# Optimization experiments

Hardware: AMD Instinct MI355X
Metric: run time of the kernel (lower is better)

The kernel has to match this reference:

```python
import jax, jax.numpy as jnp
import numpy as np

ALPHA = 0.25
GAMMA = 2.0
W_CLASS, W_BBOX, W_GIOU, W_EMBED = 1.0, 1.0, 1.0, 0.5
EPS = 1e-8


def box_cxcywh_to_xyxy(b):
    cx, cy, w, h = b[..., 0], b[..., 1], b[..., 2], b[..., 3]
    return jnp.stack([cx - 0.5 * w, cy - 0.5 * h, cx + 0.5 * w, cy + 0.5 * h], axis=-1)


def generalized_box_iou(boxes1, boxes2):
    # boxes1 [N,4], boxes2 [M,4] in xyxy -> [N,M]
    area1 = (boxes1[:, 2] - boxes1[:, 0]) * (boxes1[:, 3] - boxes1[:, 1])
    area2 = (boxes2[:, 2] - boxes2[:, 0]) * (boxes2[:, 3] - boxes2[:, 1])
    lt = jnp.maximum(boxes1[:, None, :2], boxes2[None, :, :2])  # [N,M,2]
    rb = jnp.minimum(boxes1[:, None, 2:], boxes2[None, :, 2:])
    wh = jnp.clip(rb - lt, 0.0)
    inter = wh[..., 0] * wh[..., 1]
    union = area1[:, None] + area2[None, :] - inter
    iou = inter / union
    lt_e = jnp.minimum(boxes1[:, None, :2], boxes2[None, :, :2])
    rb_e = jnp.maximum(boxes1[:, None, 2:], boxes2[None, :, 2:])
    wh_e = jnp.clip(rb_e - lt_e, 0.0)
    area_e = wh_e[..., 0] * wh_e[..., 1]
    return iou - (area_e - union) / area_e


def setup_inputs() -> dict:
    key = jax.random.key(0)
    ks = jax.random.split(key, 6)
    B, Q, C, D, M = 16, 1024, 91, 512, 1600
    pred_logits = jax.random.normal(ks[0], (B, Q, C), dtype=jnp.float32)
    pred_boxes = jax.random.uniform(ks[1], (B, Q, 4), dtype=jnp.float32)
    pred_embed = jax.random.normal(ks[2], (B, Q, D), dtype=jnp.float32)
    text_embeddings = jax.random.normal(ks[3], (C, D), dtype=jnp.float32)
    tgt_ids = jax.random.randint(ks[4], (M,), 0, C, dtype=jnp.int64 if jax.config.jax_enable_x64 else jnp.int32)
    tgt_bbox = jax.random.uniform(ks[5], (M, 4), dtype=jnp.float32)
    return {
        'pred_logits': pred_logits,
        'pred_boxes': pred_boxes,
        'pred_embed': pred_embed,
        'text_embeddings': text_embeddings,
        'tgt_ids': tgt_ids,
        'tgt_bbox': tgt_bbox,
    }


def reference(pred_logits, pred_boxes, pred_embed, text_embeddings, tgt_ids, tgt_bbox):
    B, Q, _ = pred_logits.shape
    N = B * Q
    # --- focal class cost on gathered target-class columns: [N, M]
    logits = pred_logits.reshape(N, -1)
    p = jax.nn.sigmoid(logits[:, tgt_ids])
    pos_cost = ALPHA * (1.0 - p) ** GAMMA * (-jnp.log(p + EPS))
    neg_cost = (1.0 - ALPHA) * p ** GAMMA * (-jnp.log(1.0 - p + EPS))
    cost_class = pos_cost - neg_cost
    # --- L1 box cost (cdist, p=1): [N, M]
    out_bbox = pred_boxes.reshape(N, 4)
    cost_bbox = jnp.sum(jnp.abs(out_bbox[:, None, :] - tgt_bbox[None, :, :]), axis=-1)
    # --- GIoU cost: [N, M]
    cost_giou = -generalized_box_iou(box_cxcywh_to_xyxy(out_bbox), box_cxcywh_to_xyxy(tgt_bbox))
    # --- embedding cosine cost: [N, M]
    v = pred_embed.reshape(N, -1)
    v = v / jnp.linalg.norm(v, axis=1, keepdims=True)
    te = text_embeddings[tgt_ids]  # [M, D]
    cost_embed = 1.0 - v @ te.T
    C = W_BBOX * cost_bbox + W_CLASS * cost_class + W_GIOU * cost_giou + W_EMBED * cost_embed
    return C.reshape(B, Q, -1)
```

## Files before the change

kernel.cpp:

```cpp
#include <hip/hip_runtime.h>
#include <hip/hip_bf16.h>

using bf16x8 = __attribute__((ext_vector_type(8))) short;
using f32x4  = __attribute__((ext_vector_type(4))) float;
using f32x2  = __attribute__((ext_vector_type(2))) float;

__device__ __forceinline__ unsigned short f2bf(float x) {
    unsigned int u = __float_as_uint(x);
    return (unsigned short)((u + 0x7FFFu + ((u >> 16) & 1u)) >> 16);
}

__global__ __launch_bounds__(256)
void k_prep(const float* __restrict__ te, unsigned short* __restrict__ te_bf) {
    const int r = blockIdx.x;
    for (int i = threadIdx.x; i < 512; i += 256) {
        const float v = (r < 91) ? te[(size_t)r * 512 + i] : 0.f;
        te_bf[(size_t)r * 512 + i] = f2bf(v);
    }
}

__device__ __forceinline__ float cost_core(
    float px0, float py0, float px1, float py1,
    float pcx, float pcy, float pw, float ph, float pa,
    float tx0, float ty0, float tx1, float ty1,
    float tcx, float tcy, float tw, float th, float ta, float cc)
{
    float res, t0, t1, t2, t3, t4, t5;
    asm("v_min_f32 %[t0], %[px1], %[tx1]\n\t"
        "v_max_f32 %[t1], %[px0], %[tx0]\n\t"
        "v_sub_f32 %[t0], %[t0], %[t1]\n\t"
        "v_min_f32 %[t1], %[py1], %[ty1]\n\t"
        "v_max_f32 %[t2], %[py0], %[ty0]\n\t"
        "v_sub_f32 %[t1], %[t1], %[t2]\n\t"
        "v_max_f32 %[t2], 0, %[t0]\n\t"
        "v_max_f32 %[t3], 0, %[t1]\n\t"
        "v_mul_f32 %[t4], %[t2], %[t3]\n\t"
        "v_add_f32 %[t2], %[pw], %[tw]\n\t"
        "v_sub_f32 %[t2], %[t2], %[t0]\n\t"
        "v_add_f32 %[t3], %[ph], %[th]\n\t"
        "v_sub_f32 %[t3], %[t3], %[t1]\n\t"
        "v_mul_f32 %[t0], %[t2], %[t3]\n\t"
        "v_add_f32 %[t1], %[pa], %[ta]\n\t"
        "v_sub_f32 %[t1], %[t1], %[t4]\n\t"
        "v_sub_f32 %[t2], %[t0], %[t1]\n\t"
        "v_mul_f32 %[t3], %[t1], %[t2]\n\t"
        "v_fma_f32 %[t2], %[t4], %[t0], -%[t3]\n\t"
        "v_mul_f32 %[t3], %[t1], %[t0]\n\t"
        "v_rcp_f32 %[t3], %[t3]\n\t"
        "v_sub_f32 %[t0], %[pcx], %[tcx]\n\t"
        "v_sub_f32 %[t1], %[pcy], %[tcy]\n\t"
        "v_add_f32 %[t4], |%[t0]|, |%[t1]|\n\t"
        "v_sub_f32 %[t0], %[pw], %[tw]\n\t"
        "v_sub_f32 %[t1], %[ph], %[th]\n\t"
        "v_add_f32 %[t5], |%[t0]|, |%[t1]|\n\t"
        "v_add_f32 %[t4], %[t4], %[t5]\n\t"
        "v_add_f32 %[t4], %[t4], %[cc]\n\t"
        "v_fma_f32 %[res], -%[t2], %[t3], %[t4]"
        : [res]"=v"(res), [t0]"=&v"(t0), [t1]"=&v"(t1), [t2]"=&v"(t2),
          [t3]"=&v"(t3), [t4]"=&v"(t4), [t5]"=&v"(t5)
        : [px0]"v"(px0), [py0]"v"(py0), [px1]"v"(px1), [py1]"v"(py1),
          [pcx]"v"(pcx), [pcy]"v"(pcy), [pw]"v"(pw), [ph]"v"(ph), [pa]"v"(pa),
          [tx0]"v"(tx0), [ty0]"v"(ty0), [tx1]"v"(tx1), [ty1]"v"(ty1),
          [tcx]"v"(tcx), [tcy]"v"(tcy), [tw]"v"(tw), [th]"v"(th), [ta]"v"(ta),
          [cc]"v"(cc));
    return res;
}

__global__ __launch_bounds__(256, 5)
void k_fused(const float* __restrict__ logits,
             const float* __restrict__ pboxes,
             const float* __restrict__ embed,
             const unsigned short* __restrict__ te_bf,
             const int* __restrict__ tids,
             const float* __restrict__ tboxes,
             float* __restrict__ out)
{
    __shared__ float accs[4][1536];
    __shared__ float sq_s[4][16];
    __shared__ float cc_s[1536];
    __shared__ float p_s[16 * 12];

    const int tid  = threadIdx.x;
    const int lane = tid & 63;
    const int wv   = tid >> 6;
    const int r16  = lane & 15;
    const int q    = lane >> 4;
    const int n0   = blockIdx.x * 16;

    if (tid < 16) {
        const float4 b = *(const float4*)(pboxes + (size_t)(n0 + tid) * 4);
        float* p = &p_s[tid * 12];
        p[0] = b.x; p[1] = b.y; p[2] = b.z; p[3] = b.w;
        p[4] = __builtin_fmaf(-0.5f, b.z, b.x);
        p[5] = __builtin_fmaf(-0.5f, b.w, b.y);
        p[6] = __builtin_fmaf( 0.5f, b.z, b.x);
        p[7] = __builtin_fmaf( 0.5f, b.w, b.y);
        p[8] = b.z * b.w;
    }

    const float* arow = embed + (size_t)(n0 + r16) * 512 + wv * 128 + q * 8;
    float4 A[8];
#pragma unroll
    for (int ks = 0; ks < 4; ++ks) {
        A[2 * ks]     = *(const float4*)(arow + ks * 32);
        A[2 * ks + 1] = *(const float4*)(arow + ks * 32 + 4);
    }

    float sumsq = 0.f;
    union { unsigned int uw[4]; bf16x8 v; } cvt[4];
#pragma unroll
    for (int ks = 0; ks < 4; ++ks) {
        const float4 a0 = A[2 * ks], a1 = A[2 * ks + 1];
        sumsq = __builtin_fmaf(a0.x, a0.x, sumsq);
        sumsq = __builtin_fmaf(a0.y, a0.y, sumsq);
        sumsq = __builtin_fmaf(a0.z, a0.z, sumsq);
        sumsq = __builtin_fmaf(a0.w, a0.w, sumsq);
        sumsq = __builtin_fmaf(a1.x, a1.x, sumsq);
        sumsq = __builtin_fmaf(a1.y, a1.y, sumsq);
        sumsq = __builtin_fmaf(a1.z, a1.z, sumsq);
        sumsq = __builtin_fmaf(a1.w, a1.w, sumsq);
        asm("v_cvt_pk_bf16_f32 %0, %1, %2" : "=v"(cvt[ks].uw[0]) : "v"(a0.x), "v"(a0.y));
        asm("v_cvt_pk_bf16_f32 %0, %1, %2" : "=v"(cvt[ks].uw[1]) : "v"(a0.z), "v"(a0.w));
        asm("v_cvt_pk_bf16_f32 %0, %1, %2" : "=v"(cvt[ks].uw[2]) : "v"(a1.x), "v"(a1.y));
        asm("v_cvt_pk_bf16_f32 %0, %1, %2" : "=v"(cvt[ks].uw[3]) : "v"(a1.z), "v"(a1.w));
    }

    f32x4 acc[6];
#pragma unroll
    for (int ct = 0; ct < 6; ++ct) {
        const bf16x8* bbase = (const bf16x8*)(te_bf + (size_t)(ct * 16 + r16) * 512
                                              + wv * 128 + q * 8);
        const bf16x8 b0 = bbase[0], b1 = bbase[4], b2 = bbase[8], b3 = bbase[12];
        f32x4 a = (f32x4){0.f, 0.f, 0.f, 0.f};
        a = __builtin_amdgcn_mfma_f32_16x16x32_bf16(cvt[0].v, b0, a, 0, 0, 0);
        a = __builtin_amdgcn_mfma_f32_16x16x32_bf16(cvt[1].v, b1, a, 0, 0, 0);
        a = __builtin_amdgcn_mfma_f32_16x16x32_bf16(cvt[2].v, b2, a, 0, 0, 0);
        a = __builtin_amdgcn_mfma_f32_16x16x32_bf16(cvt[3].v, b3, a, 0, 0, 0);
        acc[ct] = a;
    }

    sumsq += __shfl_xor(sumsq, 16);
    sumsq += __shfl_xor(sumsq, 32);
    if (lane < 16) sq_s[wv][r16] = sumsq;

#pragma unroll
    for (int ct = 0; ct < 6; ++ct)
#pragma unroll
        for (int j = 0; j < 4; ++j)
            accs[wv][(q * 4 + j) * 96 + ct * 16 + r16] = acc[ct][j];
    __syncthreads();

#pragma unroll
    for (int i = 0; i < 6; ++i) {
        const int e = tid + i * 256;
        const int row = e / 96, col = e - row * 96;
        float v = 0.f;
        if (col < 91) {
            const float dot = accs[0][e] + accs[1][e] + accs[2][e] + accs[3][e];
            const float rn = rsqrtf(sq_s[0][row] + sq_s[1][row]
                                  + sq_s[2][row] + sq_s[3][row]);
            const float x = logits[(size_t)(n0 + row) * 91 + col];
            const float p = 1.f / (1.f + __expf(-x));
            const float pos = 0.25f * (1.f - p) * (1.f - p) * (-__logf(p + 1e-8f));
            const float neg = 0.75f * p * p * (-__logf(1.f - p + 1e-8f));
            v = (pos - neg) + 0.5f - 0.5f * dot * rn;
        }
        cc_s[e] = v;
    }
    __syncthreads();

    const int r4 = wv * 4;
    float4 P0r[4], P1r[4];
    float  par[4];
#pragma unroll
    for (int r = 0; r < 4; ++r) {
        const float* pr = &p_s[(r4 + r) * 12];
        P0r[r] = *(const float4*)pr;
        P1r[r] = *(const float4*)(pr + 4);
        par[r] = pr[8];
    }

#pragma unroll
    for (int mc = 0; mc < 13; ++mc) {
        const int m  = mc * 128 + lane * 2;
        const bool valid = (m < 1600);
        const int mr = valid ? m : 1598;

        const float4 b0 = *(const float4*)(tboxes + (size_t)mr * 4);
        const float4 b1 = *(const float4*)(tboxes + (size_t)(mr + 1) * 4);
        const int2  idv = *(const int2*)(tids + mr);
        const int ids[2] = {idv.x, idv.y};

        float tcx[2], tcy[2], tw[2], th[2];
        float tx0[2], ty0[2], tx1[2], ty1[2], ta[2];
        const float4 bb[2] = {b0, b1};
#pragma unroll
        for (int j = 0; j < 2; ++j) {
            tcx[j] = bb[j].x; tcy[j] = bb[j].y; tw[j] = bb[j].z; th[j] = bb[j].w;
            tx0[j] = __builtin_fmaf(-0.5f, tw[j], tcx[j]);
            ty0[j] = __builtin_fmaf(-0.5f, th[j], tcy[j]);
            tx1[j] = __builtin_fmaf( 0.5f, tw[j], tcx[j]);
            ty1[j] = __builtin_fmaf( 0.5f, th[j], tcy[j]);
            ta[j]  = tw[j] * th[j];
        }

#pragma unroll
        for (int r = 0; r < 4; ++r) {
            const int nl = r4 + r;
            const float* ccrow = &cc_s[nl * 96];
            float res[2];
#pragma unroll
            for (int j = 0; j < 2; ++j) {
                res[j] = cost_core(P1r[r].x, P1r[r].y, P1r[r].z, P1r[r].w,
                                   P0r[r].x, P0r[r].y, P0r[r].z, P0r[r].w, par[r],
                                   tx0[j], ty0[j], tx1[j], ty1[j],
                                   tcx[j], tcy[j], tw[j], th[j], ta[j],
                                   ccrow[ids[j]]);
            }
            if (valid) {
                f32x2 r2 = {res[0], res[1]};
                *(f32x2*)(out + (size_t)(n0 + nl) * 1600 + m) = r2;
            }
        }
    }
}

extern "C" void kernel_launch(void* const* d_in, const int* in_sizes, int n_in,
                              void* d_out, int out_size, void* d_ws, size_t ws_size,
                              hipStream_t stream) {
    const float* pred_logits = (const float*)d_in[0];
    const float* pred_boxes  = (const float*)d_in[1];
    const float* pred_embed  = (const float*)d_in[2];
    const float* text_emb    = (const float*)d_in[3];
    const int*   tgt_ids     = (const int*)d_in[4];
    const float* tgt_bbox    = (const float*)d_in[5];
    float* out = (float*)d_out;

    unsigned short* te_bf = (unsigned short*)d_ws;

    k_prep<<<96, 256, 0, stream>>>(text_emb, te_bf);
    k_fused<<<1024, 256, 0, stream>>>(pred_logits, pred_boxes, pred_embed,
                                      te_bf, tgt_ids, tgt_bbox, out);
}
```

Baseline: 51.47 us.

## Process two 16-row tiles per block and prefetch the second tile's inputs

Each block now handles 32 prediction rows as two sequential 16-row tiles, halving the grid to 512 blocks. The embedding and logits for the second tile are loaded while the first tile's output phase runs, to hide global load latency behind the store-heavy box-cost loop. Launch bounds drop from 5 to 2 blocks per SM, which permits more registers for the extra prefetch buffers. The risks are lower occupancy, an extra barrier per tile, and fewer blocks to spread across the CUs.

Measured after the change: 53.42 us. 1.04x slower.

```diff
diff --git a/kernel.cpp b/kernel.cpp
--- a/kernel.cpp
+++ b/kernel.cpp
@@ -66,7 +66,7 @@
     return res;
 }
 
-__global__ __launch_bounds__(256, 5)
+__global__ __launch_bounds__(256, 2)
 void k_fused(const float* __restrict__ logits,
              const float* __restrict__ pboxes,
              const float* __restrict__ embed,
@@ -78,17 +78,17 @@
     __shared__ float accs[4][1536];
     __shared__ float sq_s[4][16];
     __shared__ float cc_s[1536];
-    __shared__ float p_s[16 * 12];
+    __shared__ float p_s[32 * 12];
 
     const int tid  = threadIdx.x;
     const int lane = tid & 63;
     const int wv   = tid >> 6;
     const int r16  = lane & 15;
     const int q    = lane >> 4;
-    const int n0   = blockIdx.x * 16;
-
-    if (tid < 16) {
-        const float4 b = *(const float4*)(pboxes + (size_t)(n0 + tid) * 4);
+    const int nb   = blockIdx.x * 32;
+
+    if (tid < 32) {
+        const float4 b = *(const float4*)(pboxes + (size_t)(nb + tid) * 4);
         float* p = &p_s[tid * 12];
         p[0] = b.x; p[1] = b.y; p[2] = b.z; p[3] = b.w;
         p[4] = __builtin_fmaf(-0.5f, b.z, b.x);
@@ -98,130 +98,160 @@
         p[8] = b.z * b.w;
     }
 
-    const float* arow = embed + (size_t)(n0 + r16) * 512 + wv * 128 + q * 8;
-    float4 A[8];
-#pragma unroll
-    for (int ks = 0; ks < 4; ++ks) {
-        A[2 * ks]     = *(const float4*)(arow + ks * 32);
-        A[2 * ks + 1] = *(const float4*)(arow + ks * 32 + 4);
-    }
-
-    float sumsq = 0.f;
-    union { unsigned int uw[4]; bf16x8 v; } cvt[4];
-#pragma unroll
-    for (int ks = 0; ks < 4; ++ks) {
-        const float4 a0 = A[2 * ks], a1 = A[2 * ks + 1];
-        sumsq = __builtin_fmaf(a0.x, a0.x, sumsq);
-        sumsq = __builtin_fmaf(a0.y, a0.y, sumsq);
-        sumsq = __builtin_fmaf(a0.z, a0.z, sumsq);
-        sumsq = __builtin_fmaf(a0.w, a0.w, sumsq);
-        sumsq = __builtin_fmaf(a1.x, a1.x, sumsq);
-        sumsq = __builtin_fmaf(a1.y, a1.y, sumsq);
-        sumsq = __builtin_fmaf(a1.z, a1.z, sumsq);
-        sumsq = __builtin_fmaf(a1.w, a1.w, sumsq);
-        asm("v_cvt_pk_bf16_f32 %0, %1, %2" : "=v"(cvt[ks].uw[0]) : "v"(a0.x), "v"(a0.y));
-        asm("v_cvt_pk_bf16_f32 %0, %1, %2" : "=v"(cvt[ks].uw[1]) : "v"(a0.z), "v"(a0.w));
-        asm("v_cvt_pk_bf16_f32 %0, %1, %2" : "=v"(cvt[ks].uw[2]) : "v"(a1.x), "v"(a1.y));
-        asm("v_cvt_pk_bf16_f32 %0, %1, %2" : "=v"(cvt[ks].uw[3]) : "v"(a1.z), "v"(a1.w));
-    }
-
-    f32x4 acc[6];
-#pragma unroll
-    for (int ct = 0; ct < 6; ++ct) {
-        const bf16x8* bbase = (const bf16x8*)(te_bf + (size_t)(ct * 16 + r16) * 512
-                                              + wv * 128 + q * 8);
-        const bf16x8 b0 = bbase[0], b1 = bbase[4], b2 = bbase[8], b3 = bbase[12];
-        f32x4 a = (f32x4){0.f, 0.f, 0.f, 0.f};
-        a = __builtin_amdgcn_mfma_f32_16x16x32_bf16(cvt[0].v, b0, a, 0, 0, 0);
-        a = __builtin_amdgcn_mfma_f32_16x16x32_bf16(cvt[1].v, b1, a, 0, 0, 0);
-        a = __builtin_amdgcn_mfma_f32_16x16x32_bf16(cvt[2].v, b2, a, 0, 0, 0);
-        a = __builtin_amdgcn_mfma_f32_16x16x32_bf16(cvt[3].v, b3, a, 0, 0, 0);
-        acc[ct] = a;
-    }
-
-    sumsq += __shfl_xor(sumsq, 16);
-    sumsq += __shfl_xor(sumsq, 32);
-    if (lane < 16) sq_s[wv][r16] = sumsq;
-
-#pragma unroll
-    for (int ct = 0; ct < 6; ++ct)
-#pragma unroll
-        for (int j = 0; j < 4; ++j)
-            accs[wv][(q * 4 + j) * 96 + ct * 16 + r16] = acc[ct][j];
-    __syncthreads();
-
-#pragma unroll
-    for (int i = 0; i < 6; ++i) {
-        const int e = tid + i * 256;
-        const int row = e / 96, col = e - row * 96;
-        float v = 0.f;
-        if (col < 91) {
-            const float dot = accs[0][e] + accs[1][e] + accs[2][e] + accs[3][e];
-            const float rn = rsqrtf(sq_s[0][row] + sq_s[1][row]
-                                  + sq_s[2][row] + sq_s[3][row]);
-            const float x = logits[(size_t)(n0 + row) * 91 + col];
-            const float p = 1.f / (1.f + __expf(-x));
-            const float pos = 0.25f * (1.f - p) * (1.f - p) * (-__logf(p + 1e-8f));
-            const float neg = 0.75f * p * p * (-__logf(1.f - p + 1e-8f));
-            v = (pos - neg) + 0.5f - 0.5f * dot * rn;
-        }
-        cc_s[e] = v;
-    }
-    __syncthreads();
-
-    const int r4 = wv * 4;
-    float4 P0r[4], P1r[4];
-    float  par[4];
-#pragma unroll
-    for (int r = 0; r < 4; ++r) {
-        const float* pr = &p_s[(r4 + r) * 12];
-        P0r[r] = *(const float4*)pr;
-        P1r[r] = *(const float4*)(pr + 4);
-        par[r] = pr[8];
-    }
-
-#pragma unroll
-    for (int mc = 0; mc < 13; ++mc) {
-        const int m  = mc * 128 + lane * 2;
-        const bool valid = (m < 1600);
-        const int mr = valid ? m : 1598;
-
-        const float4 b0 = *(const float4*)(tboxes + (size_t)mr * 4);
-        const float4 b1 = *(const float4*)(tboxes + (size_t)(mr + 1) * 4);
-        const int2  idv = *(const int2*)(tids + mr);
-        const int ids[2] = {idv.x, idv.y};
-
-        float tcx[2], tcy[2], tw[2], th[2];
-        float tx0[2], ty0[2], tx1[2], ty1[2], ta[2];
-        const float4 bb[2] = {b0, b1};
-#pragma unroll
-        for (int j = 0; j < 2; ++j) {
-            tcx[j] = bb[j].x; tcy[j] = bb[j].y; tw[j] = bb[j].z; th[j] = bb[j].w;
-            tx0[j] = __builtin_fmaf(-0.5f, tw[j], tcx[j]);
-            ty0[j] = __builtin_fmaf(-0.5f, th[j], tcy[j]);
-            tx1[j] = __builtin_fmaf( 0.5f, tw[j], tcx[j]);
-            ty1[j] = __builtin_fmaf( 0.5f, th[j], tcy[j]);
-            ta[j]  = tw[j] * th[j];
-        }
-
+    float4 A[2][8];
+    float  lg[2][6];
+    {
+        const float* arow = embed + (size_t)(nb + r16) * 512 + wv * 128 + q * 8;
+#pragma unroll
+        for (int ks = 0; ks < 4; ++ks) {
+            A[0][2 * ks]     = *(const float4*)(arow + ks * 32);
+            A[0][2 * ks + 1] = *(const float4*)(arow + ks * 32 + 4);
+        }
+#pragma unroll
+        for (int i = 0; i < 6; ++i) {
+            const int e = tid + i * 256;
+            const int row = e / 96, col = e - row * 96;
+            lg[0][i] = (col < 91) ? logits[(size_t)(nb + row) * 91 + col] : 0.f;
+        }
+    }
+
+#pragma unroll
+    for (int tt = 0; tt < 2; ++tt) {
+        const int n0 = nb + tt * 16;
+
+        float sumsq = 0.f;
+        union { unsigned int uw[4]; bf16x8 v; } cvt[4];
+#pragma unroll
+        for (int ks = 0; ks < 4; ++ks) {
+            const float4 a0 = A[tt][2 * ks], a1 = A[tt][2 * ks + 1];
+            sumsq = __builtin_fmaf(a0.x, a0.x, sumsq);
+            sumsq = __builtin_fmaf(a0.y, a0.y, sumsq);
+            sumsq = __builtin_fmaf(a0.z, a0.z, sumsq);
+            sumsq = __builtin_fmaf(a0.w, a0.w, sumsq);
+            sumsq = __builtin_fmaf(a1.x, a1.x, sumsq);
+            sumsq = __builtin_fmaf(a1.y, a1.y, sumsq);
+            sumsq = __builtin_fmaf(a1.z, a1.z, sumsq);
+            sumsq = __builtin_fmaf(a1.w, a1.w, sumsq);
+            asm("v_cvt_pk_bf16_f32 %0, %1, %2" : "=v"(cvt[ks].uw[0]) : "v"(a0.x), "v"(a0.y));
+            asm("v_cvt_pk_bf16_f32 %0, %1, %2" : "=v"(cvt[ks].uw[1]) : "v"(a0.z), "v"(a0.w));
+            asm("v_cvt_pk_bf16_f32 %0, %1, %2" : "=v"(cvt[ks].uw[2]) : "v"(a1.x), "v"(a1.y));
+            asm("v_cvt_pk_bf16_f32 %0, %1, %2" : "=v"(cvt[ks].uw[3]) : "v"(a1.z), "v"(a1.w));
+        }
+
+        f32x4 acc[6];
+#pragma unroll
+        for (int ct = 0; ct < 6; ++ct) {
+            const bf16x8* bbase = (const bf16x8*)(te_bf + (size_t)(ct * 16 + r16) * 512
+                                                  + wv * 128 + q * 8);
+            const bf16x8 b0 = bbase[0], b1 = bbase[4], b2 = bbase[8], b3 = bbase[12];
+            f32x4 a = (f32x4){0.f, 0.f, 0.f, 0.f};
+            a = __builtin_amdgcn_mfma_f32_16x16x32_bf16(cvt[0].v, b0, a, 0, 0, 0);
+            a = __builtin_amdgcn_mfma_f32_16x16x32_bf16(cvt[1].v, b1, a, 0, 0, 0);
+            a = __builtin_amdgcn_mfma_f32_16x16x32_bf16(cvt[2].v, b2, a, 0, 0, 0);
+            a = __builtin_amdgcn_mfma_f32_16x16x32_bf16(cvt[3].v, b3, a, 0, 0, 0);
+            acc[ct] = a;
+        }
+
+        sumsq += __shfl_xor(sumsq, 16);
+        sumsq += __shfl_xor(sumsq, 32);
+        if (lane < 16) sq_s[wv][r16] = sumsq;
+
+#pragma unroll
+        for (int ct = 0; ct < 6; ++ct)
+#pragma unroll
+            for (int j = 0; j < 4; ++j)
+                accs[wv][(q * 4 + j) * 96 + ct * 16 + r16] = acc[ct][j];
+        __syncthreads();
+
+#pragma unroll
+        for (int i = 0; i < 6; ++i) {
+            const int e = tid + i * 256;
+            const int row = e / 96, col = e - row * 96;
+            float v = 0.f;
+            if (col < 91) {
+                const float dot = accs[0][e] + accs[1][e] + accs[2][e] + accs[3][e];
+                const float rn = rsqrtf(sq_s[0][row] + sq_s[1][row]
+                                      + sq_s[2][row] + sq_s[3][row]);
+                const float x = lg[tt][i];
+                const float p = 1.f / (1.f + __expf(-x));
+                const float pos = 0.25f * (1.f - p) * (1.f - p) * (-__logf(p + 1e-8f));
+                const float neg = 0.75f * p * p * (-__logf(1.f - p + 1e-8f));
+                v = (pos - neg) + 0.5f - 0.5f * dot * rn;
+            }
+            cc_s[e] = v;
+        }
+        __syncthreads();
+
+        if (tt == 0) {
+            const float* arow = embed + (size_t)(nb + 16 + r16) * 512 + wv * 128 + q * 8;
+#pragma unroll
+            for (int ks = 0; ks < 4; ++ks) {
+                A[1][2 * ks]     = *(const float4*)(arow + ks * 32);
+                A[1][2 * ks + 1] = *(const float4*)(arow + ks * 32 + 4);
+            }
+#pragma unroll
+            for (int i = 0; i < 6; ++i) {
+                const int e = tid + i * 256;
+                const int row = e / 96, col = e - row * 96;
+                lg[1][i] = (col < 91) ? logits[(size_t)(nb + 16 + row) * 91 + col] : 0.f;
+            }
+        }
+
+        const int r4 = wv * 4;
+        float4 P0r[4], P1r[4];
+        float  par[4];
 #pragma unroll
         for (int r = 0; r < 4; ++r) {
-            const int nl = r4 + r;
-            const float* ccrow = &cc_s[nl * 96];
-            float res[2];
+            const float* pr = &p_s[(tt * 16 + r4 + r) * 12];
+            P0r[r] = *(const float4*)pr;
+            P1r[r] = *(const float4*)(pr + 4);
+            par[r] = pr[8];
+        }
+
+#pragma unroll
+        for (int mc = 0; mc < 13; ++mc) {
+            const int m  = mc * 128 + lane * 2;
+            const bool valid = (m < 1600);
+            const int mr = valid ? m : 1598;
+
+            const float4 b0 = *(const float4*)(tboxes + (size_t)mr * 4);
+            const float4 b1 = *(const float4*)(tboxes + (size_t)(mr + 1) * 4);
+            const int2  idv = *(const int2*)(tids + mr);
+            const int ids[2] = {idv.x, idv.y};
+
+            float tcx[2], tcy[2], tw[2], th[2];
+            float tx0[2], ty0[2], tx1[2], ty1[2], ta[2];
+            const float4 bb[2] = {b0, b1};
 #pragma unroll
             for (int j = 0; j < 2; ++j) {
-                res[j] = cost_core(P1r[r].x, P1r[r].y, P1r[r].z, P1r[r].w,
-                                   P0r[r].x, P0r[r].y, P0r[r].z, P0r[r].w, par[r],
-                                   tx0[j], ty0[j], tx1[j], ty1[j],
-                                   tcx[j], tcy[j], tw[j], th[j], ta[j],
-                                   ccrow[ids[j]]);
-            }
-            if (valid) {
-                f32x2 r2 = {res[0], res[1]};
-                *(f32x2*)(out + (size_t)(n0 + nl) * 1600 + m) = r2;
-            }
-        }
+                tcx[j] = bb[j].x; tcy[j] = bb[j].y; tw[j] = bb[j].z; th[j] = bb[j].w;
+                tx0[j] = __builtin_fmaf(-0.5f, tw[j], tcx[j]);
+                ty0[j] = __builtin_fmaf(-0.5f, th[j], tcy[j]);
+                tx1[j] = __builtin_fmaf( 0.5f, tw[j], tcx[j]);
+                ty1[j] = __builtin_fmaf( 0.5f, th[j], tcy[j]);
+                ta[j]  = tw[j] * th[j];
+            }
+
+#pragma unroll
+            for (int r = 0; r < 4; ++r) {
+                const int nl = r4 + r;
+                const float* ccrow = &cc_s[nl * 96];
+                float res[2];
+#pragma unroll
+                for (int j = 0; j < 2; ++j) {
+                    res[j] = cost_core(P1r[r].x, P1r[r].y, P1r[r].z, P1r[r].w,
+                                       P0r[r].x, P0r[r].y, P0r[r].z, P0r[r].w, par[r],
+                                       tx0[j], ty0[j], tx1[j], ty1[j],
+                                       tcx[j], tcy[j], tw[j], th[j], ta[j],
+                                       ccrow[ids[j]]);
+                }
+                if (valid) {
+                    f32x2 r2 = {res[0], res[1]};
+                    *(f32x2*)(out + (size_t)(n0 + nl) * 1600 + m) = r2;
+                }
+            }
+        }
+        __syncthreads();
     }
 }
 
@@ -239,6 +269,6 @@
     unsigned short* te_bf = (unsigned short*)d_ws;
 
     k_prep<<<96, 256, 0, stream>>>(text_emb, te_bf);
-    k_fused<<<1024, 256, 0, stream>>>(pred_logits, pred_boxes, pred_embed,
-                                      te_bf, tgt_ids, tgt_bbox, out);
-}
+    k_fused<<<512, 256, 0, stream>>>(pred_logits, pred_boxes, pred_embed,
+                                     te_bf, tgt_ids, tgt_bbox, out);
+}
```

## Stage embedding tile through LDS via direct global-to-LDS loads and prefetch logits

Applied to the files above, without the earlier changes.

Loads the block's 16x512 embedding tile into shared memory with global_load_lds in fully contiguous 16-byte chunks, instead of strided per-thread float4 global reads, then reads the MFMA fragments from LDS. Logits are prefetched into registers early so their latency overlaps the embedding load. The LDS staging buffer is unioned with the accumulator buffer, and launch bounds drop from 5 to 4 blocks per CU to fit the larger shared footprint. This adds an extra barrier and lowers occupancy in exchange for coalesced loads.

Measured after the change: 52.27 us. No clear change (+1.6%).

```diff
diff --git a/kernel.cpp b/kernel.cpp
--- a/kernel.cpp
+++ b/kernel.cpp
@@ -8,6 +8,12 @@
 __device__ __forceinline__ unsigned short f2bf(float x) {
     unsigned int u = __float_as_uint(x);
     return (unsigned short)((u + 0x7FFFu + ((u >> 16) & 1u)) >> 16);
+}
+
+__device__ __forceinline__ void gload_lds16(const float* g, float* l) {
+    __builtin_amdgcn_global_load_lds(
+        (__attribute__((address_space(1))) const void*)(g),
+        (__attribute__((address_space(3))) void*)(l), 16, 0, 0);
 }
 
 __global__ __launch_bounds__(256)
@@ -66,7 +72,7 @@
     return res;
 }
 
-__global__ __launch_bounds__(256, 5)
+__global__ __launch_bounds__(256, 4)
 void k_fused(const float* __restrict__ logits,
              const float* __restrict__ pboxes,
              const float* __restrict__ embed,
@@ -75,7 +81,11 @@
              const float* __restrict__ tboxes,
              float* __restrict__ out)
 {
-    __shared__ float accs[4][1536];
+    union U {
+        float abuf[16 * 512];
+        float accs[4][1536];
+    };
+    __shared__ U u;
     __shared__ float sq_s[4][16];
     __shared__ float cc_s[1536];
     __shared__ float p_s[16 * 12];
@@ -86,6 +96,13 @@
     const int r16  = lane & 15;
     const int q    = lane >> 4;
     const int n0   = blockIdx.x * 16;
+
+    const float* tbase = embed + (size_t)n0 * 512;
+#pragma unroll
+    for (int i = 0; i < 8; ++i) {
+        const int c = wv * 8 + i;
+        gload_lds16(tbase + c * 256 + lane * 4, &u.abuf[c * 256]);
+    }
 
     if (tid < 16) {
         const float4 b = *(const float4*)(pboxes + (size_t)(n0 + tid) * 4);
@@ -97,20 +114,32 @@
         p[7] = __builtin_fmaf( 0.5f, b.w, b.y);
         p[8] = b.z * b.w;
     }
-
-    const float* arow = embed + (size_t)(n0 + r16) * 512 + wv * 128 + q * 8;
-    float4 A[8];
-#pragma unroll
-    for (int ks = 0; ks < 4; ++ks) {
-        A[2 * ks]     = *(const float4*)(arow + ks * 32);
-        A[2 * ks + 1] = *(const float4*)(arow + ks * 32 + 4);
-    }
+    float lg[6];
+#pragma unroll
+    for (int i = 0; i < 6; ++i) {
+        const int e = tid + i * 256;
+        const int row = e / 96, col = e - row * 96;
+        lg[i] = (col < 91) ? logits[(size_t)(n0 + row) * 91 + col] : 0.f;
+    }
+
+    __syncthreads();
+
+    float4 F[8];
+    {
+        const float* ar = &u.abuf[r16 * 512 + wv * 128 + q * 8];
+#pragma unroll
+        for (int ks = 0; ks < 4; ++ks) {
+            F[2 * ks]     = *(const float4*)(ar + ks * 32);
+            F[2 * ks + 1] = *(const float4*)(ar + ks * 32 + 4);
+        }
+    }
+    __syncthreads();
 
     float sumsq = 0.f;
     union { unsigned int uw[4]; bf16x8 v; } cvt[4];
 #pragma unroll
     for (int ks = 0; ks < 4; ++ks) {
-        const float4 a0 = A[2 * ks], a1 = A[2 * ks + 1];
+        const float4 a0 = F[2 * ks], a1 = F[2 * ks + 1];
         sumsq = __builtin_fmaf(a0.x, a0.x, sumsq);
         sumsq = __builtin_fmaf(a0.y, a0.y, sumsq);
         sumsq = __builtin_fmaf(a0.z, a0.z, sumsq);
@@ -147,7 +176,7 @@
     for (int ct = 0; ct < 6; ++ct)
 #pragma unroll
         for (int j = 0; j < 4; ++j)
-            accs[wv][(q * 4 + j) * 96 + ct * 16 + r16] = acc[ct][j];
+            u.accs[wv][(q * 4 + j) * 96 + ct * 16 + r16] = acc[ct][j];
     __syncthreads();
 
 #pragma unroll
@@ -156,10 +185,11 @@
         const int row = e / 96, col = e - row * 96;
         float v = 0.f;
         if (col < 91) {
-            const float dot = accs[0][e] + accs[1][e] + accs[2][e] + accs[3][e];
+            const float dot = u.accs[0][e] + u.accs[1][e]
+                            + u.accs[2][e] + u.accs[3][e];
             const float rn = rsqrtf(sq_s[0][row] + sq_s[1][row]
                                   + sq_s[2][row] + sq_s[3][row]);
-            const float x = logits[(size_t)(n0 + row) * 91 + col];
+            const float x = lg[i];
             const float p = 1.f / (1.f + __expf(-x));
             const float pos = 0.25f * (1.f - p) * (1.f - p) * (-__logf(p + 1e-8f));
             const float neg = 0.75f * p * p * (-__logf(1.f - p + 1e-8f));
```
